# Kernel optimization log

Hardware: AMD Instinct MI355X
Metric: run time of the kernel (lower is better)

## Reference

```python
import jax, jax.numpy as jnp
import numpy as np


def setup_inputs() -> dict:
    key = jax.random.key(0)
    kq, kk, kv = jax.random.split(key, 3)
    S, D = 8192, 128
    return {
        "Q": jax.random.normal(kq, (S, D), dtype=jnp.float32),
        "K": jax.random.normal(kk, (S, D), dtype=jnp.float32),
        "V": jax.random.normal(kv, (S, D), dtype=jnp.float32),
    }


def reference(Q, K, V):
    d_k = Q.shape[-1]
    scale = 1.0 / jnp.sqrt(jnp.asarray(d_k, Q.dtype))
    scores = (Q @ K.T) * scale          # [S, S]
    attn = jax.nn.softmax(scores, axis=-1)
    return attn @ V                     # [S, Dv]
```

## Files before the change

### kernel.cpp

```cpp
#include <hip/hip_runtime.h>
#include <hip/hip_bf16.h>
#include <hip/hip_fp16.h>
#include <math.h>

typedef __attribute__((ext_vector_type(8))) short short8;
typedef __attribute__((ext_vector_type(16))) float f32x16;
typedef __attribute__((ext_vector_type(4))) unsigned short ushort4v;

#define S 8192
#define D 128
#define QBLK 128
#define KVB 32

__device__ __forceinline__ unsigned short f2bf(float f) {
    unsigned int x = __float_as_uint(f);
    unsigned int r = x + 0x7fffu + ((x >> 16) & 1u);
    return (unsigned short)(r >> 16);
}

__device__ __forceinline__ unsigned int cvtpk(float a, float b) {
    unsigned int r;
    asm("v_cvt_pk_bf16_f32 %0, %1, %2" : "=v"(r) : "v"(a), "v"(b));
    return r;
}

__device__ __forceinline__ float fexp2(float x) { return __builtin_amdgcn_exp2f(x); }

__device__ __forceinline__ void gl_lds16(const unsigned short* g, unsigned short* l) {
    __builtin_amdgcn_global_load_lds(
        (const __attribute__((address_space(1))) unsigned int*)g,
        (__attribute__((address_space(3))) unsigned int*)l, 16, 0, 0);
}

__device__ __forceinline__ void plswap(unsigned int& a, unsigned int& b, int hi) {
#if __has_builtin(__builtin_amdgcn_permlane32_swap)
    auto r = __builtin_amdgcn_permlane32_swap((int)a, (int)b, false, false);
    a = (unsigned int)r[0];
    b = (unsigned int)r[1];
#else
    unsigned int xa = (unsigned int)__shfl_xor((int)a, 32, 64);
    unsigned int xb = (unsigned int)__shfl_xor((int)b, 32, 64);
    unsigned int na = hi ? xb : a;
    unsigned int nb = hi ? b : xa;
    a = na; b = nb;
#endif
}

union W4 { unsigned int u[4]; short8 v; };

__global__ __launch_bounds__(256) void prep_kv(const float* __restrict__ K,
                                               const float* __restrict__ V,
                                               unsigned short* __restrict__ Kb,
                                               unsigned short* __restrict__ Vt) {
    __shared__ unsigned short T[64][72];
    const float scale = 0.12751743022854459f;
    int s0 = blockIdx.x * 64, d0 = blockIdx.y * 64;
    int tr = threadIdx.x >> 4, tc = (threadIdx.x & 15) * 4;
#pragma unroll
    for (int p = 0; p < 4; ++p) {
        int r = p * 16 + tr;
        float4 kf = *reinterpret_cast<const float4*>(K + (size_t)(s0 + r) * D + d0 + tc);
        ushort4v ko = { f2bf(kf.x * scale), f2bf(kf.y * scale),
                        f2bf(kf.z * scale), f2bf(kf.w * scale) };
        *reinterpret_cast<ushort4v*>(Kb + (size_t)(s0 + r) * D + d0 + tc) = ko;
        float4 v = *reinterpret_cast<const float4*>(V + (size_t)(s0 + r) * D + d0 + tc);
        ushort4v vo = { f2bf(v.x), f2bf(v.y), f2bf(v.z), f2bf(v.w) };
        *reinterpret_cast<ushort4v*>(&T[r][tc]) = vo;
    }
    __syncthreads();
#pragma unroll
    for (int p = 0; p < 4; ++p) {
        int dr = p * 16 + tr;
        ushort4v o = { T[tc + 0][dr], T[tc + 1][dr], T[tc + 2][dr], T[tc + 3][dr] };
        *reinterpret_cast<ushort4v*>(Vt + (size_t)(d0 + dr) * S + s0 + tc) = o;
    }
}

#define QKOP(acc, kc) (acc) = __builtin_amdgcn_mfma_f32_32x32x16_bf16(              \
    *reinterpret_cast<const short8*>(                                               \
        &Kl[(size_t)c31 * 128 + (((2 * (kc) + hi) ^ (c31 & 15)) * 8)]),             \
    qf[kc], (acc), 0, 0, 0)

#define PVOP(oo, pp, dt, off) (oo) = __builtin_amdgcn_mfma_f32_32x32x16_bf16(       \
    (pp).v,                                                                          \
    *reinterpret_cast<const short8*>(                                               \
        &Vl[((dt) * 32 + c31) * 32 + ((((off) + hi) ^ sw) * 8)]),                    \
    (oo), 0, 0, 0)

#define SMEX(PD0, PD1)                                                               \
    {                                                                                \
        float e[16];                                                                 \
        _Pragma("unroll")                                                            \
        for (int i = 0; i < 16; ++i) e[i] = fexp2(sa[i] + sb[i]);                    \
        float t0 = (e[0] + e[1]) + (e[2] + e[3]);                                    \
        float t1 = (e[4] + e[5]) + (e[6] + e[7]);                                    \
        float t2 = (e[8] + e[9]) + (e[10] + e[11]);                                  \
        float t3 = (e[12] + e[13]) + (e[14] + e[15]);                                \
        l_r += (t0 + t1) + (t2 + t3);                                                \
        unsigned int wd[8];                                                          \
        _Pragma("unroll")                                                            \
        for (int u = 0; u < 8; ++u) wd[u] = cvtpk(e[2 * u], e[2 * u + 1]);           \
        plswap(wd[0], wd[2], hi); plswap(wd[1], wd[3], hi);                          \
        plswap(wd[4], wd[6], hi); plswap(wd[5], wd[7], hi);                          \
        PD0.u[0] = wd[0]; PD0.u[1] = wd[1]; PD0.u[2] = wd[2]; PD0.u[3] = wd[3];      \
        PD1.u[0] = wd[4]; PD1.u[1] = wd[5]; PD1.u[2] = wd[6]; PD1.u[3] = wd[7];      \
    }

#define STAGE_K(RING) do {                                                           \
    gl_lds16(kg[0], &Klds[RING][(w * 2 + 0) * 512]); kg[0] += (size_t)KVB * D;       \
    gl_lds16(kg[1], &Klds[RING][(w * 2 + 1) * 512]); kg[1] += (size_t)KVB * D;       \
} while (0)

#define STAGE_V(RING) do {                                                           \
    gl_lds16(vg[0], &Vlds[RING][(w * 2 + 0) * 512]); vg[0] += KVB;                   \
    gl_lds16(vg[1], &Vlds[RING][(w * 2 + 1) * 512]); vg[1] += KVB;                   \
} while (0)

#define PHASE_BARRIER() do {                                                         \
    asm volatile("s_waitcnt vmcnt(0)" ::: "memory");                                 \
    __builtin_amdgcn_s_barrier();                                                    \
    __builtin_amdgcn_sched_barrier(0);                                               \
} while (0)

#define SUBTILE(KR, VR, PP0, PP1, QQ0, QQ1)                                          \
    {                                                                                \
        const unsigned short* Kl = Klds[KR];                                         \
        const unsigned short* Vl = Vlds[VR];                                         \
        f32x16 sa, sb;                                                               \
        _Pragma("unroll")                                                            \
        for (int i = 0; i < 16; ++i) { sa[i] = 0.f; sb[i] = 0.f; }                   \
        __builtin_amdgcn_s_setprio(1);                                               \
        QKOP(sa, 0); QKOP(sb, 1);                                                    \
        PVOP(o0, PP0, 0, 0); QKOP(sa, 2); PVOP(o0, PP1, 0, 2);                       \
        QKOP(sb, 3); PVOP(o1, PP0, 1, 0); QKOP(sa, 4); PVOP(o1, PP1, 1, 2);          \
        QKOP(sb, 5); PVOP(o2, PP0, 2, 0); QKOP(sa, 6); PVOP(o2, PP1, 2, 2);          \
        QKOP(sb, 7); PVOP(o3, PP0, 3, 0); PVOP(o3, PP1, 3, 2);                       \
        __builtin_amdgcn_s_setprio(0);                                               \
        SMEX(QQ0, QQ1);                                                              \
    }

#define SUBTILE_NOPV(KR, QQ0, QQ1)                                                   \
    {                                                                                \
        const unsigned short* Kl = Klds[KR];                                         \
        f32x16 sa, sb;                                                               \
        _Pragma("unroll")                                                            \
        for (int i = 0; i < 16; ++i) { sa[i] = 0.f; sb[i] = 0.f; }                   \
        __builtin_amdgcn_s_setprio(1);                                               \
        QKOP(sa, 0); QKOP(sb, 1); QKOP(sa, 2); QKOP(sb, 3);                          \
        QKOP(sa, 4); QKOP(sb, 5); QKOP(sa, 6); QKOP(sb, 7);                          \
        __builtin_amdgcn_s_setprio(0);                                               \
        SMEX(QQ0, QQ1);                                                              \
    }

__global__ __launch_bounds__(256, 2) void attn_fwd(
    const float* __restrict__ Q, const unsigned short* __restrict__ Kb,
    const unsigned short* __restrict__ Vtg, float* __restrict__ out,
    __half* __restrict__ wsO, float* __restrict__ wsL, int split)
{
    __shared__ __attribute__((aligned(16))) unsigned short Klds[4][KVB * D];
    __shared__ __attribute__((aligned(16))) unsigned short Vlds[4][D * KVB];

    const int tid  = threadIdx.x;
    const int w    = tid >> 6;
    const int lane = tid & 63;
    const int hi   = lane >> 5;
    const int c31  = lane & 31;
    const int sw   = (c31 >> 1) & 3;
    const int bid  = blockIdx.x;
    const int sp   = bid % split;
    const int qb   = bid / split;
    const int chunk  = S / split;
    const int kv0    = sp * chunk;
    const int ntiles = chunk / KVB;

    short8 qf[8];
    {
        const float* qrow = Q + (size_t)(qb * QBLK + w * 32 + c31) * D;
#pragma unroll
        for (int kc = 0; kc < 8; ++kc) {
            float4 x = *reinterpret_cast<const float4*>(qrow + kc * 16 + hi * 8);
            float4 y = *reinterpret_cast<const float4*>(qrow + kc * 16 + hi * 8 + 4);
            W4 u;
            u.u[0] = cvtpk(x.x, x.y); u.u[1] = cvtpk(x.z, x.w);
            u.u[2] = cvtpk(y.x, y.y); u.u[3] = cvtpk(y.z, y.w);
            qf[kc] = u.v;
        }
    }

    const unsigned short* kg[2];
    const unsigned short* vg[2];
#pragma unroll
    for (int i = 0; i < 2; ++i) {
        int krow = w * 8 + i * 4 + (lane >> 4);
        int kch  = (lane & 15) ^ (krow & 15);
        kg[i] = Kb + (size_t)(kv0 + krow) * D + kch * 8;
        int vrow = w * 32 + i * 16 + (lane >> 2);
        int vch  = (lane & 3) ^ ((vrow >> 1) & 3);
        vg[i] = Vtg + (size_t)vrow * S + kv0 + vch * 8;
    }

    f32x16 o0, o1, o2, o3;
#pragma unroll
    for (int i = 0; i < 16; ++i) { o0[i] = 0.f; o1[i] = 0.f; o2[i] = 0.f; o3[i] = 0.f; }
    float l_r = 0.f;
    W4 pX0, pX1, pY0, pY1;

    STAGE_K(0); STAGE_K(1); STAGE_V(0);

    PHASE_BARRIER();
    STAGE_K(2); STAGE_K(3);
    STAGE_V(1); STAGE_V(2);
    SUBTILE_NOPV(0, pY0, pY1);
    SUBTILE(1, 0, pY0, pY1, pX0, pX1);

    const int npair = ntiles / 4 - 1;
#pragma unroll 1
    for (int j = 0; j < npair; ++j) {
        PHASE_BARRIER();
        STAGE_K(0); STAGE_K(1);
        STAGE_V(3); STAGE_V(0);
        SUBTILE(2, 1, pX0, pX1, pY0, pY1);
        SUBTILE(3, 2, pY0, pY1, pX0, pX1);
        PHASE_BARRIER();
        STAGE_K(2); STAGE_K(3);
        STAGE_V(1); STAGE_V(2);
        SUBTILE(0, 3, pX0, pX1, pY0, pY1);
        SUBTILE(1, 0, pY0, pY1, pX0, pX1);
    }

    PHASE_BARRIER();
    STAGE_V(3);
    SUBTILE(2, 1, pX0, pX1, pY0, pY1);
    SUBTILE(3, 2, pY0, pY1, pX0, pX1);

    PHASE_BARRIER();
    {
        const unsigned short* Vl = Vlds[3];
        __builtin_amdgcn_s_setprio(1);
        PVOP(o0, pX0, 0, 0); PVOP(o0, pX1, 0, 2);
        PVOP(o1, pX0, 1, 0); PVOP(o1, pX1, 1, 2);
        PVOP(o2, pX0, 2, 0); PVOP(o2, pX1, 2, 2);
        PVOP(o3, pX0, 3, 0); PVOP(o3, pX1, 3, 2);
        __builtin_amdgcn_s_setprio(0);
    }

    float l_tot = l_r + __shfl_xor(l_r, 32, 64);
    if (split == 1) {
#pragma unroll
        for (int reg = 0; reg < 16; ++reg) {
            int crow = (reg & 3) + 8 * (reg >> 2) + 4 * hi;
            float lr  = __shfl(l_tot, crow, 64);
            float inv = 1.f / lr;
            size_t rb = (size_t)(qb * QBLK + w * 32 + crow) * D;
            out[rb +  0 + c31] = o0[reg] * inv;
            out[rb + 32 + c31] = o1[reg] * inv;
            out[rb + 64 + c31] = o2[reg] * inv;
            out[rb + 96 + c31] = o3[reg] * inv;
        }
    } else {
        __half* Opart = wsO + (size_t)(qb * split + sp) * (QBLK * D);
#pragma unroll
        for (int reg = 0; reg < 16; ++reg) {
            int crow = (reg & 3) + 8 * (reg >> 2) + 4 * hi;
            size_t rb = (size_t)(w * 32 + crow) * D;
            Opart[rb +  0 + c31] = __float2half(o0[reg]);
            Opart[rb + 32 + c31] = __float2half(o1[reg]);
            Opart[rb + 64 + c31] = __float2half(o2[reg]);
            Opart[rb + 96 + c31] = __float2half(o3[reg]);
        }
        if (hi == 0)
            wsL[(size_t)(qb * split + sp) * QBLK + w * 32 + c31] = l_tot;
    }
}

__global__ void attn_combine(const __half* __restrict__ wsO,
                             const float* __restrict__ wsL,
                             float* __restrict__ out, int split)
{
    int idx = blockIdx.x * blockDim.x + threadIdx.x;
    if (idx >= S * D) return;
    int row = idx >> 7, col = idx & 127;
    int qb = row >> 7, rloc = row & 127;
    float acc = 0.f, L = 0.f;
    for (int s = 0; s < split; ++s) {
        size_t b = (size_t)(qb * split + s);
        acc += __half2float(wsO[b * (QBLK * D) + (size_t)rloc * D + col]);
        L   += wsL[b * QBLK + rloc];
    }
    out[idx] = acc / L;
}

extern "C" void kernel_launch(void* const* d_in, const int* in_sizes, int n_in,
                              void* d_out, int out_size, void* d_ws, size_t ws_size,
                              hipStream_t stream) {
    const float* Q = (const float*)d_in[0];
    const float* K = (const float*)d_in[1];
    const float* V = (const float*)d_in[2];
    float* out = (float*)d_out;

    size_t base = 2ull * S * D * sizeof(unsigned short);
    int split = 1;
    for (int sp = 8; sp >= 2; sp >>= 1) {
        size_t need = base + (size_t)sp * S * D * sizeof(__half)
                    + (size_t)sp * S * sizeof(float);
        if (ws_size >= need) { split = sp; break; }
    }

    unsigned short* Kb = (unsigned short*)d_ws;
    unsigned short* Vt = Kb + (size_t)S * D;
    __half* wsO = (__half*)(Vt + (size_t)S * D);
    float* wsL = (float*)(wsO + (size_t)split * S * D);

    prep_kv<<<dim3(S / 64, D / 64), 256, 0, stream>>>(K, V, Kb, Vt);
    attn_fwd<<<(S / QBLK) * split, 256, 0, stream>>>(Q, Kb, Vt, out, wsO, wsL, split);
    if (split > 1)
        attn_combine<<<(S * D + 255) / 256, 256, 0, stream>>>(wsO, wsL, out, split);
}
```

Measured before the change: 59.44 us.

## Use 8-wave 256-row Q blocks, split up to 16, vectorize combine

Doubles the Q block to 256 rows processed by 8 waves of 512 threads, so each K/V tile staged in LDS is reused by twice as many query rows. Each wave now issues one global-to-LDS load per tile instead of two. The split-K factor may now go up to 16 to keep enough blocks in flight. The combine kernel is vectorized to read 8 halfs and write two float4 per thread. In exchange, occupancy drops to one 512-thread block per CU, and the larger split adds more partial-output workspace traffic.

```diff
diff --git a/kernel.cpp b/kernel.cpp
--- a/kernel.cpp
+++ b/kernel.cpp
@@ -6,10 +6,11 @@
 typedef __attribute__((ext_vector_type(8))) short short8;
 typedef __attribute__((ext_vector_type(16))) float f32x16;
 typedef __attribute__((ext_vector_type(4))) unsigned short ushort4v;
+typedef __attribute__((ext_vector_type(4))) unsigned int uint4v;
 
 #define S 8192
 #define D 128
-#define QBLK 128
+#define QBLK 256
 #define KVB 32
 
 __device__ __forceinline__ unsigned short f2bf(float f) {
@@ -107,13 +108,11 @@
     }
 
 #define STAGE_K(RING) do {                                                           \
-    gl_lds16(kg[0], &Klds[RING][(w * 2 + 0) * 512]); kg[0] += (size_t)KVB * D;       \
-    gl_lds16(kg[1], &Klds[RING][(w * 2 + 1) * 512]); kg[1] += (size_t)KVB * D;       \
+    gl_lds16(kgp, &Klds[RING][w * 512]); kgp += (size_t)KVB * D;                     \
 } while (0)
 
 #define STAGE_V(RING) do {                                                           \
-    gl_lds16(vg[0], &Vlds[RING][(w * 2 + 0) * 512]); vg[0] += KVB;                   \
-    gl_lds16(vg[1], &Vlds[RING][(w * 2 + 1) * 512]); vg[1] += KVB;                   \
+    gl_lds16(vgp, &Vlds[RING][w * 512]); vgp += KVB;                                 \
 } while (0)
 
 #define PHASE_BARRIER() do {                                                         \
@@ -152,7 +151,7 @@
         SMEX(QQ0, QQ1);                                                              \
     }
 
-__global__ __launch_bounds__(256, 2) void attn_fwd(
+__global__ __launch_bounds__(512, 1) void attn_fwd_b8(
     const float* __restrict__ Q, const unsigned short* __restrict__ Kb,
     const unsigned short* __restrict__ Vtg, float* __restrict__ out,
     __half* __restrict__ wsO, float* __restrict__ wsL, int split)
@@ -187,17 +186,12 @@
         }
     }
 
-    const unsigned short* kg[2];
-    const unsigned short* vg[2];
-#pragma unroll
-    for (int i = 0; i < 2; ++i) {
-        int krow = w * 8 + i * 4 + (lane >> 4);
-        int kch  = (lane & 15) ^ (krow & 15);
-        kg[i] = Kb + (size_t)(kv0 + krow) * D + kch * 8;
-        int vrow = w * 32 + i * 16 + (lane >> 2);
-        int vch  = (lane & 3) ^ ((vrow >> 1) & 3);
-        vg[i] = Vtg + (size_t)vrow * S + kv0 + vch * 8;
-    }
+    int krow = w * 4 + (lane >> 4);
+    int kch  = (lane & 15) ^ (krow & 15);
+    const unsigned short* kgp = Kb + (size_t)(kv0 + krow) * D + kch * 8;
+    int vrow = w * 16 + (lane >> 2);
+    int vch  = (lane & 3) ^ ((vrow >> 1) & 3);
+    const unsigned short* vgp = Vtg + (size_t)vrow * S + kv0 + vch * 8;
 
     f32x16 o0, o1, o2, o3;
 #pragma unroll
@@ -278,16 +272,34 @@
                              float* __restrict__ out, int split)
 {
     int idx = blockIdx.x * blockDim.x + threadIdx.x;
-    if (idx >= S * D) return;
-    int row = idx >> 7, col = idx & 127;
-    int qb = row >> 7, rloc = row & 127;
-    float acc = 0.f, L = 0.f;
+    if (idx >= S * D / 8) return;
+    int row = idx >> 4;
+    int g   = (idx & 15) * 8;
+    int qb = row >> 8, rloc = row & 255;
+    float acc[8];
+#pragma unroll
+    for (int i = 0; i < 8; ++i) acc[i] = 0.f;
+    float L = 0.f;
     for (int s = 0; s < split; ++s) {
         size_t b = (size_t)(qb * split + s);
-        acc += __half2float(wsO[b * (QBLK * D) + (size_t)rloc * D + col]);
-        L   += wsL[b * QBLK + rloc];
-    }
-    out[idx] = acc / L;
+        const __half* p = wsO + b * (QBLK * D) + (size_t)rloc * D + g;
+        uint4v u = *reinterpret_cast<const uint4v*>(p);
+#pragma unroll
+        for (int i = 0; i < 4; ++i) {
+            unsigned int wbits = u[i];
+            __half2 h = *reinterpret_cast<__half2*>(&wbits);
+            float2 f = __half22float2(h);
+            acc[2 * i]     += f.x;
+            acc[2 * i + 1] += f.y;
+        }
+        L += wsL[b * QBLK + rloc];
+    }
+    float inv = 1.f / L;
+    size_t ob = (size_t)row * D + g;
+    float4 w0 = { acc[0] * inv, acc[1] * inv, acc[2] * inv, acc[3] * inv };
+    float4 w1 = { acc[4] * inv, acc[5] * inv, acc[6] * inv, acc[7] * inv };
+    *reinterpret_cast<float4*>(out + ob)     = w0;
+    *reinterpret_cast<float4*>(out + ob + 4) = w1;
 }
 
 extern "C" void kernel_launch(void* const* d_in, const int* in_sizes, int n_in,
@@ -300,7 +312,7 @@
 
     size_t base = 2ull * S * D * sizeof(unsigned short);
     int split = 1;
-    for (int sp = 8; sp >= 2; sp >>= 1) {
+    for (int sp = 16; sp >= 2; sp >>= 1) {
         size_t need = base + (size_t)sp * S * D * sizeof(__half)
                     + (size_t)sp * S * sizeof(float);
         if (ws_size >= need) { split = sp; break; }
@@ -312,7 +324,7 @@
     float* wsL = (float*)(wsO + (size_t)split * S * D);
 
     prep_kv<<<dim3(S / 64, D / 64), 256, 0, stream>>>(K, V, Kb, Vt);
-    attn_fwd<<<(S / QBLK) * split, 256, 0, stream>>>(Q, Kb, Vt, out, wsO, wsL, split);
+    attn_fwd_b8<<<(S / QBLK) * split, 512, 0, stream>>>(Q, Kb, Vt, out, wsO, wsL, split);
     if (split > 1)
-        attn_combine<<<(S * D + 255) / 256, 256, 0, stream>>>(wsO, wsL, out, split);
-}
+        attn_combine<<<(S * D / 8 + 255) / 256, 256, 0, stream>>>(wsO, wsL, out, split);
+}
```

Result: slower. 64.06 us (+7.8%).
